# Kernel tuning notes

Hardware: AMD Instinct MI355X
Metric: run time of the kernel (lower is better)

The kernel has to match this reference:

```python
import jax, jax.numpy as jnp
import numpy as np

B, S, D, H, FF = 16, 384, 768, 12, 3072
DH = D // H


def layer_norm(x, g, b, eps=1e-5):
    m = jnp.mean(x, axis=-1, keepdims=True)
    v = jnp.mean((x - m) ** 2, axis=-1, keepdims=True)
    return (x - m) * jax.lax.rsqrt(v + eps) * g + b


def setup_inputs() -> dict:
    key = jax.random.key(0)
    ks = jax.random.split(key, 12)
    s = 0.02
    return {
        "x": jax.random.normal(ks[0], (B, S, D), dtype=jnp.float32),
        "pe": jax.random.normal(ks[1], (2 * S - 1, D), dtype=jnp.float32) * s,  # relative-position table for offsets -(S-1)..(S-1)
        "Wq": jax.random.normal(ks[2], (D, D), dtype=jnp.float32) * s,
        "Wk": jax.random.normal(ks[3], (D, D), dtype=jnp.float32) * s,
        "Wv": jax.random.normal(ks[4], (D, D), dtype=jnp.float32) * s,
        "Wr": jax.random.normal(ks[5], (D, D), dtype=jnp.float32) * s,
        "u": jax.random.normal(ks[6], (H, DH), dtype=jnp.float32) * s,  # content bias (Transformer-XL)
        "v": jax.random.normal(ks[7], (H, DH), dtype=jnp.float32) * s,  # position bias
        "Wo": jax.random.normal(ks[8], (D, D), dtype=jnp.float32) * s,  # attn_ff output projection
        "ln1_g": jnp.ones((D,), dtype=jnp.float32),
        "ln1_b": jnp.zeros((D,), dtype=jnp.float32),
        "ln2_g": jnp.ones((D,), dtype=jnp.float32),
        "ln2_b": jnp.zeros((D,), dtype=jnp.float32),
        "W1": jax.random.normal(ks[9], (D, FF), dtype=jnp.float32) * s,
        "b1": jnp.zeros((FF,), dtype=jnp.float32),
        "W2": jax.random.normal(ks[10], (FF, D), dtype=jnp.float32) * s,
        "b2": jnp.zeros((D,), dtype=jnp.float32),
    }


def reference(x, pe, Wq, Wk, Wv, Wr, u, v, Wo, ln1_g, ln1_b, ln2_g, ln2_b, W1, b1, W2, b2):
    # --- relative-position multi-head self-attention (FLAT / Transformer-XL style) ---
    q = (x @ Wq).reshape(B, S, H, DH)
    k = (x @ Wk).reshape(B, S, H, DH)
    val = (x @ Wv).reshape(B, S, H, DH)
    # project relative table once, then gather per (i, j) offset
    r = (pe @ Wr).reshape(2 * S - 1, H, DH)
    idx = jnp.arange(S)[:, None] - jnp.arange(S)[None, :] + (S - 1)  # [S,S], offset i-j shifted
    rel = r[idx]  # [S,S,H,DH]
    A_C = jnp.einsum("bqhd,bkhd->bhqk", q + u, k)
    B_D = jnp.einsum("bqhd,qkhd->bhqk", q + v, rel)
    scores = (A_C + B_D) * (1.0 / np.sqrt(DH))  # scaled=True
    p = jax.nn.softmax(scores, axis=-1)
    attn = jnp.einsum("bhqk,bkhd->bqhd", p, val).reshape(B, S, D) @ Wo
    # layer_postprocess_sequence = 'an': add residual, then layernorm
    x1 = layer_norm(x + attn, ln1_g, ln1_b)
    # --- FFN (relu) with 'an' postprocess ---
    ff = jax.nn.relu(x1 @ W1 + b1) @ W2 + b2
    return layer_norm(x1 + ff, ln2_g, ln2_b)
```

## Files before the change

### kernel.cpp

```cpp
#include <hip/hip_runtime.h>

typedef unsigned short u16;
typedef __attribute__((ext_vector_type(8))) short short8;
typedef __attribute__((ext_vector_type(4))) float floatx4;

#define B_  16
#define S_  384
#define D_  768
#define H_  12
#define DH_ 64
#define FF_ 3072

__device__ __forceinline__ float b2f(u16 h) { return __uint_as_float(((unsigned)h) << 16); }
__device__ __forceinline__ u16 f2b(float f) {
  unsigned u = __float_as_uint(f);
  u += 0x7fffu + ((u >> 16) & 1u);
  return (u16)(u >> 16);
}

__device__ __forceinline__ void gload16(const u16* g, u16* l) {
  __builtin_amdgcn_global_load_lds(
      (const __attribute__((address_space(1))) unsigned int*)g,
      (__attribute__((address_space(3))) unsigned int*)l, 16, 0, 0);
}

__global__ __launch_bounds__(256) void fill_sentinel(u16* out, int n) {
  int i = blockIdx.x * 256 + threadIdx.x;
  if (i < n) out[i] = 0x42DE;
}

__global__ __launch_bounds__(256) void detect_dtype(const u16* __restrict__ x, int* flag) {
  __shared__ int cnt;
  if (threadIdx.x == 0) cnt = 0;
  __syncthreads();
  int c = 0;
  for (int i = threadIdx.x; i < 8192; i += 256) {
    const unsigned e = (x[i] >> 7) & 0xFFu;
    if (e >= 0xC0u) ++c;
  }
  atomicAdd(&cnt, c);
  __syncthreads();
  if (threadIdx.x == 0) *flag = (cnt > 64) ? 1 : 0;
}

__global__ __launch_bounds__(256) void convert_in4(const void* __restrict__ src,
                                                   u16* __restrict__ dst, int n4,
                                                   const int* __restrict__ flag) {
  const int i = blockIdx.x * 256 + threadIdx.x;
  if (i >= n4) return;
  if (*flag) {
    const float4 f = ((const float4*)src)[i];
    ushort4 o;
    o.x = f2b(f.x); o.y = f2b(f.y); o.z = f2b(f.z); o.w = f2b(f.w);
    ((ushort4*)dst)[i] = o;
  } else {
    ((ushort4*)dst)[i] = ((const ushort4*)src)[i];
  }
}

__global__ __launch_bounds__(256) void convert_small(
    const void* b1, const void* ub, const void* vb, const void* b2,
    const void* g1, const void* be1, const void* g2, const void* be2,
    u16* b1c, u16* ubc, u16* vbc, u16* b2c,
    u16* g1c, u16* be1c, u16* g2c, u16* be2c, const int* __restrict__ flag) {
  const int i = blockIdx.x * 256 + threadIdx.x;
  if (i >= 8448) return;
  const void* s; u16* d; int off;
  if (i < 3072) { s = b1; d = b1c; off = i; }
  else {
    const int r = i - 3072, sg = r / 768; off = r - sg * 768;
    switch (sg) {
      case 0: s = ub;  d = ubc;  break;
      case 1: s = vb;  d = vbc;  break;
      case 2: s = b2;  d = b2c;  break;
      case 3: s = g1;  d = g1c;  break;
      case 4: s = be1; d = be1c; break;
      case 5: s = g2;  d = g2c;  break;
      default: s = be2; d = be2c; break;
    }
  }
  d[off] = (*flag) ? f2b(((const float*)s)[off]) : ((const u16*)s)[off];
}

struct TP { const void* src[7]; u16* dst[7]; };
__global__ __launch_bounds__(256) void transpose_all(TP tp, const int* __restrict__ flag) {
  __shared__ u16 t[32][33];
  const int f32 = *flag;
  const int id = blockIdx.x;
  int w, tt, R, C, bc, br;
  if (id < 2880)      { w = id / 576; tt = id % 576;  R = 768;  C = 768;  bc = (tt % 24) * 32; br = (tt / 24) * 32; }
  else if (id < 5184) { w = 5;        tt = id - 2880; R = 768;  C = 3072; bc = (tt % 96) * 32; br = (tt / 96) * 32; }
  else                { w = 6;        tt = id - 5184; R = 3072; C = 768;  bc = (tt % 24) * 32; br = (tt / 24) * 32; }
  const void* in = tp.src[w];
  u16* out = tp.dst[w];
  const int tx = threadIdx.x & 31, ty = threadIdx.x >> 5;
  for (int i = ty; i < 32; i += 8) {
    const size_t idx = (size_t)(br + i) * C + bc + tx;
    t[i][tx] = f32 ? f2b(((const float*)in)[idx]) : ((const u16*)in)[idx];
  }
  __syncthreads();
  for (int i = ty; i < 32; i += 8) out[(size_t)(bc + i) * R + br + tx] = t[tx][i];
}

enum { F_BIAS = 1, F_RELU = 2, F_RES = 4, F_QKV = 8 };

template <int TM, int TN, int WM, int WN, int FLAGS>
__global__ __launch_bounds__(256) void gemm3(
    const u16* __restrict__ A, const u16* __restrict__ Bt,
    u16* __restrict__ out0, u16* __restrict__ out1,
    u16* __restrict__ out2, u16* __restrict__ out3,
    const u16* __restrict__ bias0, const u16* __restrict__ bias1,
    const u16* __restrict__ res, int M, int N, int K) {
  constexpr int WAVES_M = TM / WM;
  constexpr int MT = WM / 16, NT = WN / 16;
  constexpr int NI = (TM + TN) / 64;
  static_assert((TM / WM) * (TN / WN) == 4, "4 waves");
  __shared__ u16 SM[2][(TM + TN) * 32];

  const int m0 = blockIdx.y * TM;
  const int n0 = blockIdx.x * TN;
  const int tid = threadIdx.x;
  const int wid = tid >> 6, lane = tid & 63;
  const int wm = (wid % WAVES_M) * WM, wn = (wid / WAVES_M) * WN;
  const int lm = lane & 15, quad = lane >> 4;

  floatx4 acc[MT][NT];
#pragma unroll
  for (int i = 0; i < MT; ++i)
#pragma unroll
    for (int j = 0; j < NT; ++j) acc[i][j] = (floatx4){0.f, 0.f, 0.f, 0.f};

  const u16* srcs[NI];
  int ldso[NI];
#pragma unroll
  for (int i = 0; i < NI; ++i) {
    const int j = wid + 4 * i;
    const int r = j * 16 + (lane >> 2);
    const int q = (lane & 3) ^ ((r >> 1) & 3);
    const u16* p;
    if (r < TM) {
      int ga = m0 + r;
      if (ga > M - 1) ga = M - 1;
      p = A + (size_t)ga * K + q * 8;
    } else {
      p = Bt + (size_t)(n0 + r - TM) * K + q * 8;
    }
    srcs[i] = p;
    ldso[i] = j * 512;
  }
  const int slot = (quad ^ ((lm >> 1) & 3)) * 8;
  int aoff[MT], boff[NT];
#pragma unroll
  for (int t = 0; t < MT; ++t) aoff[t] = (wm + t * 16 + lm) * 32 + slot;
#pragma unroll
  for (int t = 0; t < NT; ++t) boff[t] = (TM + wn + t * 16 + lm) * 32 + slot;

#pragma unroll
  for (int i = 0; i < NI; ++i) gload16(srcs[i], &SM[0][ldso[i]]);
  __syncthreads();

  int buf = 0;
  for (int k0 = 0; k0 < K; k0 += 32, buf ^= 1) {
    if (k0 + 32 < K) {
      const int koff = (k0 + 32);
#pragma unroll
      for (int i = 0; i < NI; ++i) gload16(srcs[i] + koff, &SM[buf ^ 1][ldso[i]]);
    }
    short8 af[MT], bf[NT];
#pragma unroll
    for (int t = 0; t < MT; ++t) af[t] = *(const short8*)(&SM[buf][aoff[t]]);
#pragma unroll
    for (int t = 0; t < NT; ++t) bf[t] = *(const short8*)(&SM[buf][boff[t]]);
#pragma unroll
    for (int tm = 0; tm < MT; ++tm)
#pragma unroll
      for (int tn = 0; tn < NT; ++tn)
        acc[tm][tn] = __builtin_amdgcn_mfma_f32_16x16x32_bf16(af[tm], bf[tn], acc[tm][tn], 0, 0, 0);
    __syncthreads();
  }

#pragma unroll
  for (int tm = 0; tm < MT; ++tm) {
#pragma unroll
    for (int tn = 0; tn < NT; ++tn) {
      const int gcol = n0 + wn + tn * 16 + lm;
#pragma unroll
      for (int r = 0; r < 4; ++r) {
        const int grow = m0 + wm + tm * 16 + quad * 4 + r;
        if (grow >= M) continue;
        float val = acc[tm][tn][r];
        if (FLAGS & F_QKV) {
          const int region = gcol / 768;
          const int c = gcol - region * 768;
          if (region == 0) {
            out0[(size_t)grow * 768 + c] = f2b(val + b2f(bias0[c]));
            out1[(size_t)grow * 768 + c] = f2b(val + b2f(bias1[c]));
          } else if (region == 1) {
            out2[(size_t)grow * 768 + c] = f2b(val);
          } else {
            const int bb = grow / S_, s = grow - bb * S_;
            out3[((size_t)bb * D_ + c) * S_ + s] = f2b(val);
          }
        } else {
          if (FLAGS & F_BIAS) val += b2f(bias0[gcol]);
          if (FLAGS & F_RES) val += b2f(res[(size_t)grow * N + gcol]);
          if (FLAGS & F_RELU) val = fmaxf(val, 0.f);
          out0[(size_t)grow * N + gcol] = f2b(val);
        }
      }
    }
  }
}

__global__ __launch_bounds__(256, 4) void attn_kernel(
    const u16* __restrict__ qu, const u16* __restrict__ qv,
    const u16* __restrict__ kb, const u16* __restrict__ vt,
    const u16* __restrict__ rb, u16* __restrict__ attn) {
  __shared__ float scA[16 * 388];
  __shared__ u16 Eb[16 * 408];
  __shared__ float rsum[16];

  const int id = blockIdx.x;
  const int g = id >> 3;
  const int qt = g % 24;
  const int bh = (id & 7) + 8 * (g / 24);
  const int b = bh / H_, h = bh % H_;
  const int i0 = qt * 16;
  const int tid = threadIdx.x, wid = tid >> 6, lane = tid & 63;
  const int lm = lane & 15, quad = lane >> 4;

  const size_t qrow = ((size_t)(b * S_ + i0 + lm)) * D_ + h * DH_;
  const short8 av0 = *(const short8*)(qv + qrow + quad * 8);
  const short8 av1 = *(const short8*)(qv + qrow + 32 + quad * 8);
  const short8 au0 = *(const short8*)(qu + qrow + quad * 8);
  const short8 au1 = *(const short8*)(qu + qrow + 32 + quad * 8);

  short8 r0, r1, k0, k1;
  {
    int t = i0 + wid * 16 + lm; if (t > 766) t = 766;
    const u16* p = rb + (size_t)t * D_ + h * DH_;
    r0 = *(const short8*)(p + quad * 8);
    r1 = *(const short8*)(p + 32 + quad * 8);
    const u16* q = kb + ((size_t)(b * S_ + wid * 96 + lm)) * D_ + h * DH_;
    k0 = *(const short8*)(q + quad * 8);
    k1 = *(const short8*)(q + 32 + quad * 8);
  }
#pragma unroll
  for (int i = 0; i < 7; ++i) {
    short8 nr0 = r0, nr1 = r1, nk0 = k0, nk1 = k1;
    const int ntt = wid + 4 * (i + 1);
    if (ntt < 25) {
      int t = i0 + ntt * 16 + lm; if (t > 766) t = 766;
      const u16* p = rb + (size_t)t * D_ + h * DH_;
      nr0 = *(const short8*)(p + quad * 8);
      nr1 = *(const short8*)(p + 32 + quad * 8);
    }
    if (i + 1 < 6) {
      const u16* q = kb + ((size_t)(b * S_ + (wid * 6 + i + 1) * 16 + lm)) * D_ + h * DH_;
      nk0 = *(const short8*)(q + quad * 8);
      nk1 = *(const short8*)(q + 32 + quad * 8);
    }
    const int tt = wid + 4 * i;
    if (tt < 25) {
      floatx4 e = (floatx4){0.f, 0.f, 0.f, 0.f};
      e = __builtin_amdgcn_mfma_f32_16x16x32_bf16(av0, r0, e, 0, 0, 0);
      e = __builtin_amdgcn_mfma_f32_16x16x32_bf16(av1, r1, e, 0, 0, 0);
#pragma unroll
      for (int r = 0; r < 4; ++r) Eb[(quad * 4 + r) * 408 + tt * 16 + lm] = f2b(e[r]);
    }
    if (i < 6) {
      floatx4 e = (floatx4){0.f, 0.f, 0.f, 0.f};
      e = __builtin_amdgcn_mfma_f32_16x16x32_bf16(au0, k0, e, 0, 0, 0);
      e = __builtin_amdgcn_mfma_f32_16x16x32_bf16(au1, k1, e, 0, 0, 0);
#pragma unroll
      for (int r = 0; r < 4; ++r) scA[(quad * 4 + r) * 388 + (wid * 6 + i) * 16 + lm] = e[r];
    }
    r0 = nr0; r1 = nr1; k0 = nk0; k1 = nk1;
  }
  __syncthreads();

  short8 vv[12];
  const size_t vbase = ((size_t)(b * D_ + h * DH_ + wid * 16 + lm)) * S_;
#pragma unroll
  for (int kk = 0; kk < 12; ++kk)
    vv[kk] = *(const short8*)(vt + vbase + kk * 32 + quad * 8);

  u16* p16 = (u16*)scA;
  {
    const int row = wid * 4 + quad;
    float v[24];
    float lmax = -1e30f;
#pragma unroll
    for (int cc = 0; cc < 24; ++cc) {
      const int c = lm + cc * 16;
      const float s = (scA[row * 388 + c] + b2f(Eb[row * 408 + row + 383 - c])) * 0.125f;
      v[cc] = s;
      lmax = fmaxf(lmax, s);
    }
#pragma unroll
    for (int m = 1; m < 16; m <<= 1) lmax = fmaxf(lmax, __shfl_xor(lmax, m));
    float lsum = 0.f;
#pragma unroll
    for (int cc = 0; cc < 24; ++cc) {
      const float e = __expf(v[cc] - lmax);
      p16[row * 776 + lm + cc * 16] = f2b(e);
      lsum += e;
    }
#pragma unroll
    for (int m = 1; m < 16; m <<= 1) lsum += __shfl_xor(lsum, m);
    if (lm == 0) rsum[row] = lsum;
  }
  __syncthreads();

  floatx4 o = (floatx4){0.f, 0.f, 0.f, 0.f};
#pragma unroll
  for (int kk = 0; kk < 12; ++kk) {
    const short8 af = *(const short8*)(&p16[lm * 776 + kk * 32 + quad * 8]);
    o = __builtin_amdgcn_mfma_f32_16x16x32_bf16(af, vv[kk], o, 0, 0, 0);
  }
#pragma unroll
  for (int r = 0; r < 4; ++r) {
    const int row = quad * 4 + r;
    attn[((size_t)(b * S_ + i0 + row)) * D_ + h * DH_ + wid * 16 + lm] =
        f2b(o[r] / rsum[row]);
  }
}

__global__ __launch_bounds__(256) void ln_kernel(const u16* __restrict__ y,
                                                 const u16* __restrict__ g,
                                                 const u16* __restrict__ bb,
                                                 void* __restrict__ outv,
                                                 const int* __restrict__ flag, int dual) {
  const int row = blockIdx.x * 4 + (threadIdx.x >> 6);
  const int lane = threadIdx.x & 63;
  const u16* yr = y + (size_t)row * D_;
  float vbuf[12], s = 0.f, s2 = 0.f;
#pragma unroll
  for (int i = 0; i < 12; ++i) {
    const float x = b2f(yr[lane + i * 64]);
    vbuf[i] = x;
    s += x;
    s2 += x * x;
  }
#pragma unroll
  for (int off = 32; off; off >>= 1) {
    s += __shfl_down(s, off);
    s2 += __shfl_down(s2, off);
  }
  s = __shfl(s, 0);
  s2 = __shfl(s2, 0);
  const float mean = s * (1.f / 768.f);
  const float var = s2 * (1.f / 768.f) - mean * mean;
  const float inv = rsqrtf(var + 1e-5f);
  const int f32out = dual && *flag;
#pragma unroll
  for (int i = 0; i < 12; ++i) {
    const int c = lane + i * 64;
    const float val = (vbuf[i] - mean) * inv * b2f(g[c]) + b2f(bb[c]);
    if (f32out) ((float*)outv)[(size_t)row * D_ + c] = val;
    else ((u16*)outv)[(size_t)row * D_ + c] = f2b(val);
  }
}

extern "C" void kernel_launch(void* const* d_in, const int* in_sizes, int n_in,
                              void* d_out, int out_size, void* d_ws, size_t ws_size,
                              hipStream_t stream) {
  const void* x    = d_in[0];
  const void* pe   = d_in[1];
  const void* Wq   = d_in[2];
  const void* Wk   = d_in[3];
  const void* Wv   = d_in[4];
  const void* Wr   = d_in[5];
  const void* ub   = d_in[6];
  const void* vb   = d_in[7];
  const void* Wo   = d_in[8];
  const void* ln1g = d_in[9];
  const void* ln1b = d_in[10];
  const void* ln2g = d_in[11];
  const void* ln2b = d_in[12];
  const void* W1   = d_in[13];
  const void* b1   = d_in[14];
  const void* W2   = d_in[15];
  const void* b2   = d_in[16];
  char* ws = (char*)d_ws;

  constexpr int N_X  = B_ * S_ * D_;
  constexpr int N_PE = (2 * S_ - 1) * D_;

  constexpr size_t O_W   = 0;
  constexpr size_t O_SM  = 15335424;
  constexpr size_t O_XB  = 15368192;
  constexpr size_t O_QU  = 24805376;
  constexpr size_t O_QV  = 34242560;
  constexpr size_t O_KB  = 43679744;
  constexpr size_t O_VT  = 53116928;
  constexpr size_t O_RB  = 62554112;
  constexpr size_t NEEDED = 63733760;

  if (ws_size < NEEDED) {
    fill_sentinel<<<(out_size + 255) / 256, 256, 0, stream>>>((u16*)d_out, out_size);
    return;
  }

  int* flag = (int*)(ws + O_SM);
  u16* ubc  = (u16*)(ws + O_SM + 128);
  u16* vbc  = (u16*)(ws + O_SM + 1664);
  u16* b1c  = (u16*)(ws + O_SM + 3200);
  u16* b2c  = (u16*)(ws + O_SM + 9344);
  u16* g1c  = (u16*)(ws + O_SM + 10880);
  u16* be1c = (u16*)(ws + O_SM + 12416);
  u16* g2c  = (u16*)(ws + O_SM + 13952);
  u16* be2c = (u16*)(ws + O_SM + 15488);

  u16* wtq = (u16*)(ws + O_W);
  u16* wtk = wtq + (size_t)D_ * D_;
  u16* wtv = wtk + (size_t)D_ * D_;
  u16* wtr = wtv + (size_t)D_ * D_;
  u16* wto = wtr + (size_t)D_ * D_;
  u16* wt1 = wto + (size_t)D_ * D_;
  u16* wt2 = wt1 + (size_t)D_ * FF_;

  u16* xb  = (u16*)(ws + O_XB);
  u16* quB = (u16*)(ws + O_QU);
  u16* peb = (u16*)(ws + O_QV);
  u16* qvB = (u16*)(ws + O_QV);
  u16* kbB = (u16*)(ws + O_KB);
  u16* vtB = (u16*)(ws + O_VT);
  u16* rbB = (u16*)(ws + O_RB);
  u16* atB = (u16*)d_out;
  u16* y1B = xb;
  u16* x1B = (u16*)(ws + O_VT);
  u16* ffB = xb;
  u16* y2B = x1B;

  detect_dtype<<<1, 256, 0, stream>>>((const u16*)x, flag);
  convert_in4<<<(N_X / 4 + 255) / 256, 256, 0, stream>>>(x, xb, N_X / 4, flag);
  convert_in4<<<(N_PE / 4 + 255) / 256, 256, 0, stream>>>(pe, peb, N_PE / 4, flag);
  convert_small<<<33, 256, 0, stream>>>(b1, ub, vb, b2, ln1g, ln1b, ln2g, ln2b,
                                        b1c, ubc, vbc, b2c, g1c, be1c, g2c, be2c, flag);
  TP tp;
  tp.src[0] = Wq; tp.src[1] = Wk; tp.src[2] = Wv; tp.src[3] = Wr; tp.src[4] = Wo;
  tp.src[5] = W1; tp.src[6] = W2;
  tp.dst[0] = wtq; tp.dst[1] = wtk; tp.dst[2] = wtv; tp.dst[3] = wtr; tp.dst[4] = wto;
  tp.dst[5] = wt1; tp.dst[6] = wt2;
  transpose_all<<<7488, 256, 0, stream>>>(tp, flag);

  gemm3<64, 64, 32, 32, 0><<<dim3(12, 12), 256, 0, stream>>>(
      peb, wtr, rbB, nullptr, nullptr, nullptr, nullptr, nullptr, nullptr,
      2 * S_ - 1, D_, D_);
  gemm3<128, 128, 64, 64, F_QKV><<<dim3(18, 48), 256, 0, stream>>>(
      xb, wtq, quB, qvB, kbB, vtB, ubc, vbc, nullptr, B_ * S_, 2304, D_);
  attn_kernel<<<4608, 256, 0, stream>>>(quB, qvB, kbB, vtB, rbB, atB);
  gemm3<64, 128, 32, 64, F_RES><<<dim3(6, 96), 256, 0, stream>>>(
      atB, wto, y1B, nullptr, nullptr, nullptr, nullptr, nullptr, xb, B_ * S_, D_, D_);
  ln_kernel<<<B_ * S_ / 4, 256, 0, stream>>>(y1B, g1c, be1c, x1B, flag, 0);
  gemm3<128, 128, 64, 64, F_BIAS | F_RELU><<<dim3(24, 48), 256, 0, stream>>>(
      x1B, wt1, ffB, nullptr, nullptr, nullptr, b1c, nullptr, nullptr, B_ * S_, FF_, D_);
  gemm3<64, 128, 32, 64, F_BIAS | F_RES><<<dim3(6, 96), 256, 0, stream>>>(
      ffB, wt2, y2B, nullptr, nullptr, nullptr, b2c, nullptr, x1B, B_ * S_, D_, FF_);
  ln_kernel<<<B_ * S_ / 4, 256, 0, stream>>>(y2B, g2c, be2c, d_out, flag, 1);
}
```

Before: 462.2 us.

## Process 32 query rows per attention block with 512 threads to reuse K/R tiles

The attention kernel now handles 32 query rows per block with 8 waves instead of 16 rows with 4 waves. Each loaded K and relative-position tile feeds two query sub-tiles, and adjacent query tiles share overlapping R tiles, so global reads of K and R per query row roughly halve. The register prefetch of K/R and the up-front V preload are dropped: V is now read inside the PV loop and split across waves by row group and column tile. The trade is more LDS per block, which may lower occupancy, and exposed global-load latency without prefetching.

```diff
diff --git a/kernel.cpp b/kernel.cpp
--- a/kernel.cpp
+++ b/kernel.cpp
@@ -212,88 +212,89 @@
   }
 }
 
-__global__ __launch_bounds__(256, 4) void attn_kernel(
+__global__ __launch_bounds__(512, 4) void attn_kernel(
     const u16* __restrict__ qu, const u16* __restrict__ qv,
     const u16* __restrict__ kb, const u16* __restrict__ vt,
     const u16* __restrict__ rb, u16* __restrict__ attn) {
-  __shared__ float scA[16 * 388];
-  __shared__ u16 Eb[16 * 408];
-  __shared__ float rsum[16];
+  __shared__ float scA[32 * 396];
+  __shared__ u16 Eb[32 * 424];
+  __shared__ float rsum[32];
 
   const int id = blockIdx.x;
   const int g = id >> 3;
-  const int qt = g % 24;
-  const int bh = (id & 7) + 8 * (g / 24);
+  const int qt = g % 12;
+  const int bh = (id & 7) + 8 * (g / 12);
   const int b = bh / H_, h = bh % H_;
-  const int i0 = qt * 16;
+  const int i0 = qt * 32;
   const int tid = threadIdx.x, wid = tid >> 6, lane = tid & 63;
   const int lm = lane & 15, quad = lane >> 4;
 
-  const size_t qrow = ((size_t)(b * S_ + i0 + lm)) * D_ + h * DH_;
-  const short8 av0 = *(const short8*)(qv + qrow + quad * 8);
-  const short8 av1 = *(const short8*)(qv + qrow + 32 + quad * 8);
-  const short8 au0 = *(const short8*)(qu + qrow + quad * 8);
-  const short8 au1 = *(const short8*)(qu + qrow + 32 + quad * 8);
-
-  short8 r0, r1, k0, k1;
-  {
-    int t = i0 + wid * 16 + lm; if (t > 766) t = 766;
-    const u16* p = rb + (size_t)t * D_ + h * DH_;
-    r0 = *(const short8*)(p + quad * 8);
-    r1 = *(const short8*)(p + 32 + quad * 8);
-    const u16* q = kb + ((size_t)(b * S_ + wid * 96 + lm)) * D_ + h * DH_;
-    k0 = *(const short8*)(q + quad * 8);
-    k1 = *(const short8*)(q + 32 + quad * 8);
-  }
+  const size_t qr0 = ((size_t)(b * S_ + i0 + lm)) * D_ + h * DH_;
+  const size_t qr1 = qr0 + (size_t)16 * D_;
+  const short8 qv0a = *(const short8*)(qv + qr0 + quad * 8);
+  const short8 qv0b = *(const short8*)(qv + qr0 + 32 + quad * 8);
+  const short8 qv1a = *(const short8*)(qv + qr1 + quad * 8);
+  const short8 qv1b = *(const short8*)(qv + qr1 + 32 + quad * 8);
+  const short8 qu0a = *(const short8*)(qu + qr0 + quad * 8);
+  const short8 qu0b = *(const short8*)(qu + qr0 + 32 + quad * 8);
+  const short8 qu1a = *(const short8*)(qu + qr1 + quad * 8);
+  const short8 qu1b = *(const short8*)(qu + qr1 + 32 + quad * 8);
+
 #pragma unroll
   for (int i = 0; i < 7; ++i) {
-    short8 nr0 = r0, nr1 = r1, nk0 = k0, nk1 = k1;
-    const int ntt = wid + 4 * (i + 1);
-    if (ntt < 25) {
-      int t = i0 + ntt * 16 + lm; if (t > 766) t = 766;
+    const int u = wid + 8 * i;
+    if (u >= 50) break;
+    if (u < 26) {
+      const int m = u;
+      int t = i0 + 16 * m + lm;
+      if (t > 766) t = 766;
       const u16* p = rb + (size_t)t * D_ + h * DH_;
-      nr0 = *(const short8*)(p + quad * 8);
-      nr1 = *(const short8*)(p + 32 + quad * 8);
-    }
-    if (i + 1 < 6) {
-      const u16* q = kb + ((size_t)(b * S_ + (wid * 6 + i + 1) * 16 + lm)) * D_ + h * DH_;
-      nk0 = *(const short8*)(q + quad * 8);
-      nk1 = *(const short8*)(q + 32 + quad * 8);
-    }
-    const int tt = wid + 4 * i;
-    if (tt < 25) {
-      floatx4 e = (floatx4){0.f, 0.f, 0.f, 0.f};
-      e = __builtin_amdgcn_mfma_f32_16x16x32_bf16(av0, r0, e, 0, 0, 0);
-      e = __builtin_amdgcn_mfma_f32_16x16x32_bf16(av1, r1, e, 0, 0, 0);
-#pragma unroll
-      for (int r = 0; r < 4; ++r) Eb[(quad * 4 + r) * 408 + tt * 16 + lm] = f2b(e[r]);
-    }
-    if (i < 6) {
-      floatx4 e = (floatx4){0.f, 0.f, 0.f, 0.f};
-      e = __builtin_amdgcn_mfma_f32_16x16x32_bf16(au0, k0, e, 0, 0, 0);
-      e = __builtin_amdgcn_mfma_f32_16x16x32_bf16(au1, k1, e, 0, 0, 0);
-#pragma unroll
-      for (int r = 0; r < 4; ++r) scA[(quad * 4 + r) * 388 + (wid * 6 + i) * 16 + lm] = e[r];
-    }
-    r0 = nr0; r1 = nr1; k0 = nk0; k1 = nk1;
-  }
-  __syncthreads();
-
-  short8 vv[12];
-  const size_t vbase = ((size_t)(b * D_ + h * DH_ + wid * 16 + lm)) * S_;
-#pragma unroll
-  for (int kk = 0; kk < 12; ++kk)
-    vv[kk] = *(const short8*)(vt + vbase + kk * 32 + quad * 8);
+      const short8 b0 = *(const short8*)(p + quad * 8);
+      const short8 b1 = *(const short8*)(p + 32 + quad * 8);
+      if (m <= 24) {
+        floatx4 e = (floatx4){0.f, 0.f, 0.f, 0.f};
+        e = __builtin_amdgcn_mfma_f32_16x16x32_bf16(qv0a, b0, e, 0, 0, 0);
+        e = __builtin_amdgcn_mfma_f32_16x16x32_bf16(qv0b, b1, e, 0, 0, 0);
+#pragma unroll
+        for (int r = 0; r < 4; ++r) Eb[(quad * 4 + r) * 424 + 16 * m + lm] = f2b(e[r]);
+      }
+      if (m >= 1) {
+        floatx4 e = (floatx4){0.f, 0.f, 0.f, 0.f};
+        e = __builtin_amdgcn_mfma_f32_16x16x32_bf16(qv1a, b0, e, 0, 0, 0);
+        e = __builtin_amdgcn_mfma_f32_16x16x32_bf16(qv1b, b1, e, 0, 0, 0);
+#pragma unroll
+        for (int r = 0; r < 4; ++r) Eb[(16 + quad * 4 + r) * 424 + 16 * (m - 1) + lm] = f2b(e[r]);
+      }
+    } else {
+      const int j = u - 26;
+      const u16* p = kb + ((size_t)(b * S_ + j * 16 + lm)) * D_ + h * DH_;
+      const short8 b0 = *(const short8*)(p + quad * 8);
+      const short8 b1 = *(const short8*)(p + 32 + quad * 8);
+      floatx4 e0 = (floatx4){0.f, 0.f, 0.f, 0.f};
+      e0 = __builtin_amdgcn_mfma_f32_16x16x32_bf16(qu0a, b0, e0, 0, 0, 0);
+      e0 = __builtin_amdgcn_mfma_f32_16x16x32_bf16(qu0b, b1, e0, 0, 0, 0);
+      floatx4 e1 = (floatx4){0.f, 0.f, 0.f, 0.f};
+      e1 = __builtin_amdgcn_mfma_f32_16x16x32_bf16(qu1a, b0, e1, 0, 0, 0);
+      e1 = __builtin_amdgcn_mfma_f32_16x16x32_bf16(qu1b, b1, e1, 0, 0, 0);
+#pragma unroll
+      for (int r = 0; r < 4; ++r) {
+        scA[(quad * 4 + r) * 396 + j * 16 + lm] = e0[r];
+        scA[(16 + quad * 4 + r) * 396 + j * 16 + lm] = e1[r];
+      }
+    }
+  }
+  __syncthreads();
 
   u16* p16 = (u16*)scA;
   {
     const int row = wid * 4 + quad;
+    const int rbase = row * 424 + (row & 15) + 383;
     float v[24];
     float lmax = -1e30f;
 #pragma unroll
     for (int cc = 0; cc < 24; ++cc) {
       const int c = lm + cc * 16;
-      const float s = (scA[row * 388 + c] + b2f(Eb[row * 408 + row + 383 - c])) * 0.125f;
+      const float s = (scA[row * 396 + c] + b2f(Eb[rbase - c])) * 0.125f;
       v[cc] = s;
       lmax = fmaxf(lmax, s);
     }
@@ -303,7 +304,7 @@
 #pragma unroll
     for (int cc = 0; cc < 24; ++cc) {
       const float e = __expf(v[cc] - lmax);
-      p16[row * 776 + lm + cc * 16] = f2b(e);
+      p16[row * 792 + lm + cc * 16] = f2b(e);
       lsum += e;
     }
 #pragma unroll
@@ -312,17 +313,23 @@
   }
   __syncthreads();
 
-  floatx4 o = (floatx4){0.f, 0.f, 0.f, 0.f};
-#pragma unroll
-  for (int kk = 0; kk < 12; ++kk) {
-    const short8 af = *(const short8*)(&p16[lm * 776 + kk * 32 + quad * 8]);
-    o = __builtin_amdgcn_mfma_f32_16x16x32_bf16(af, vv[kk], o, 0, 0, 0);
-  }
-#pragma unroll
-  for (int r = 0; r < 4; ++r) {
-    const int row = quad * 4 + r;
-    attn[((size_t)(b * S_ + i0 + row)) * D_ + h * DH_ + wid * 16 + lm] =
-        f2b(o[r] / rsum[row]);
+  {
+    const int rg = wid & 1, nt = wid >> 1;
+    floatx4 o = (floatx4){0.f, 0.f, 0.f, 0.f};
+    const size_t vbase = ((size_t)(b * D_ + h * DH_ + nt * 16 + lm)) * S_;
+    const int pbase = (rg * 16 + lm) * 792;
+#pragma unroll
+    for (int kk = 0; kk < 12; ++kk) {
+      const short8 af = *(const short8*)(&p16[pbase + kk * 32 + quad * 8]);
+      const short8 bv = *(const short8*)(vt + vbase + kk * 32 + quad * 8);
+      o = __builtin_amdgcn_mfma_f32_16x16x32_bf16(af, bv, o, 0, 0, 0);
+    }
+#pragma unroll
+    for (int r = 0; r < 4; ++r) {
+      const int row = rg * 16 + quad * 4 + r;
+      attn[((size_t)(b * S_ + i0 + row)) * D_ + h * DH_ + nt * 16 + lm] =
+          f2b(o[r] / rsum[row]);
+    }
   }
 }
 
@@ -450,7 +457,7 @@
       2 * S_ - 1, D_, D_);
   gemm3<128, 128, 64, 64, F_QKV><<<dim3(18, 48), 256, 0, stream>>>(
       xb, wtq, quB, qvB, kbB, vtB, ubc, vbc, nullptr, B_ * S_, 2304, D_);
-  attn_kernel<<<4608, 256, 0, stream>>>(quB, qvB, kbB, vtB, rbB, atB);
+  attn_kernel<<<2304, 512, 0, stream>>>(quB, qvB, kbB, vtB, rbB, atB);
   gemm3<64, 128, 32, 64, F_RES><<<dim3(6, 96), 256, 0, stream>>>(
       atB, wto, y1B, nullptr, nullptr, nullptr, nullptr, nullptr, xb, B_ * S_, D_, D_);
   ln_kernel<<<B_ * S_ / 4, 256, 0, stream>>>(y1B, g1c, be1c, x1B, flag, 0);
```

Result: no change. 459.5 us (-0.6%).
